# Performance work log

Hardware: AMD Instinct MI355X
Metric: run time of the kernel (lower is better)

The kernel has to match this reference:

```python
import jax, jax.numpy as jnp
import numpy as np

B_FACTOR = 4          # branching factor of the complete tree
DEPTH = 7             # levels 0..DEPTH; level DEPTH are leaves
N_NODES = (B_FACTOR ** (DEPTH + 1) - 1) // (B_FACTOR - 1)   # 21845
N_INTERNAL = (B_FACTOR ** DEPTH - 1) // (B_FACTOR - 1)      # 5461
IN_SIZE = 512
HID = 512
PARAM_SCALE = 0.02


def setup_inputs() -> dict:
    key = jax.random.key(0)
    ks = jax.random.split(key, 7)
    x = jax.random.normal(ks[0], (N_NODES, IN_SIZE), dtype=jnp.float32)
    # torch nn.Linear parameters: y = x @ W.T + b
    W_iou = jax.random.normal(ks[1], (3 * HID, IN_SIZE), dtype=jnp.float32) * PARAM_SCALE
    b_iou = jax.random.normal(ks[2], (3 * HID,), dtype=jnp.float32) * PARAM_SCALE
    W_f = jax.random.normal(ks[3], (HID, IN_SIZE), dtype=jnp.float32) * PARAM_SCALE
    b_f = jax.random.normal(ks[4], (HID,), dtype=jnp.float32) * PARAM_SCALE
    U_iou = jax.random.normal(ks[5], (3 * HID, HID), dtype=jnp.float32) * PARAM_SCALE
    U_f = jax.random.normal(ks[6], (HID, HID), dtype=jnp.float32) * PARAM_SCALE
    # children[j] = indices of the 4 children of internal node j (complete 4-ary tree)
    children = (B_FACTOR * jnp.arange(N_INTERNAL, dtype=jnp.int32)[:, None]
                + jnp.arange(1, B_FACTOR + 1, dtype=jnp.int32)[None, :])
    return {"x": x, "children": children, "W_iou": W_iou, "b_iou": b_iou,
            "W_f": W_f, "b_f": b_f, "U_iou": U_iou, "U_f": U_f}


def reference(x, children, W_iou, b_iou, W_f, b_f, U_iou, U_f):
    """Child-Sum Tree-LSTM over a complete 4-ary tree, processed level-batched
    bottom-up (equivalent to the per-node postorder recursion in the source).
    Leaves keep h = c = 0, as in the source (_forward_postorder returns early).
    NOTE: the source applies NO sigmoid to the forget gate term; we keep that.
    """
    N = x.shape[0]
    H = U_f.shape[0]
    # input-dependent parts are tree-independent: precompute once for all nodes
    wx_iou = x @ W_iou.T + b_iou          # [N, 3H]
    wx_f = x @ W_f.T + b_f                # [N, H]
    h = jnp.zeros((N, H), dtype=x.dtype)
    c = jnp.zeros_like(h)
    # level l occupies node indices [offs[l], offs[l+1]) — static constants
    offs = [(B_FACTOR ** l - 1) // (B_FACTOR - 1) for l in range(DEPTH + 2)]
    for l in range(DEPTH - 1, -1, -1):    # internal levels, deepest first
        s, e = offs[l], offs[l + 1]
        ch = children[s:e]                # [M, 4]
        h_ch = h[ch]                      # [M, 4, H] gather of child hidden states
        c_ch = c[ch]                      # [M, 4, H]
        h_sum = h_ch.sum(axis=1)          # child-sum
        iou = wx_iou[s:e] + h_sum @ U_iou.T               # [M, 3H]
        i, o, u = jnp.split(iou, 3, axis=-1)
        i = jax.nn.sigmoid(i)
        o = jax.nn.sigmoid(o)
        u = jnp.tanh(u)
        # forget term per child (no sigmoid, faithful to source)
        f = wx_f[s:e][:, None, :] + h_ch @ U_f.T          # [M, 4, H]
        c_new = i * u + (f * c_ch).sum(axis=1)            # [M, H]
        h = h.at[s:e].set(o * jnp.tanh(c_new))
        c = c.at[s:e].set(c_new)
    return h, c
```

## Files before the change

### kernel.cpp

```cpp
#include <hip/hip_runtime.h>
#include <cmath>

constexpr int N_NODES = 21845;
constexpr int N_INT   = 5461;
constexpr int HID     = 512;

typedef short  short8  __attribute__((ext_vector_type(8)));
typedef float  floatx4 __attribute__((ext_vector_type(4)));

__device__ __forceinline__ unsigned short f2bf(float f) {
    unsigned int u = __float_as_uint(f);
    u += 0x7fffu + ((u >> 16) & 1u);
    return (unsigned short)(u >> 16);
}

__global__ void prep_kernel(const float* __restrict__ x,
                            const float* __restrict__ W_iou,
                            const float* __restrict__ W_f,
                            const float* __restrict__ U_iou,
                            const float* __restrict__ U_f,
                            float* __restrict__ h_leaf,
                            float* __restrict__ c_leaf,
                            unsigned short* __restrict__ dstb,
                            unsigned* __restrict__ bar)
{
    if (blockIdx.x == 0 && threadIdx.x == 0) bar[0] = 0u;
    const size_t Z  = (size_t)(N_NODES - N_INT) * HID / 4;
    const size_t C0 = (size_t)N_INT * 512 / 4;
    const size_t C1 = C0 + 1536 * 512 / 4;
    const size_t C2 = C1 + 512 * 512 / 4;
    const size_t C3 = C2 + 1536 * 512 / 4;
    const size_t C4 = C3 + 512 * 512 / 4;
    const size_t total = 2 * Z + C4;
    size_t i = (size_t)blockIdx.x * blockDim.x + threadIdx.x;
    const size_t stride = (size_t)gridDim.x * blockDim.x;
    const float4 zz = {0.f, 0.f, 0.f, 0.f};
    for (; i < total; i += stride) {
        if (i < 2 * Z) {
            if (i < Z) ((float4*)h_leaf)[i] = zz;
            else       ((float4*)c_leaf)[i - Z] = zz;
        } else {
            size_t k = i - 2 * Z;
            const float* src; size_t off;
            if (k < C0)      { src = x;     off = k; }
            else if (k < C1) { src = W_iou; off = k - C0; }
            else if (k < C2) { src = W_f;   off = k - C1; }
            else if (k < C3) { src = U_iou; off = k - C2; }
            else             { src = U_f;   off = k - C3; }
            float4 v = ((const float4*)src)[off];
            ushort4 o;
            o.x = f2bf(v.x); o.y = f2bf(v.y); o.z = f2bf(v.z); o.w = f2bf(v.w);
            ((ushort4*)dstb)[k] = o;
        }
    }
}

#define GLD_LDS(g, l) __builtin_amdgcn_global_load_lds( \
    (const __attribute__((address_space(1))) void*)(g), \
    (__attribute__((address_space(3))) void*)(l), 16, 0, 0)

__device__ __forceinline__ void gemm_tile_128(
    const unsigned short* __restrict__ A, int Arows,
    const unsigned short* __restrict__ B,
    const float* __restrict__ bias,
    float* __restrict__ C, int ldc,
    int bm, int bn)
{
    __shared__ short8 AsV[1024];
    __shared__ short8 BsV[1024];

    const int tid  = threadIdx.x;
    const int wave = tid >> 6;
    const int lane = tid & 63;
    const int quad = lane >> 4;
    const int lr   = lane & 15;
    const int wr = (wave >> 1) * 64;
    const int wc = (wave & 1) * 64;

    floatx4 acc[4][4];
    #pragma unroll
    for (int i = 0; i < 4; ++i)
        #pragma unroll
        for (int j = 0; j < 4; ++j)
            acc[i][j] = (floatx4){0.f, 0.f, 0.f, 0.f};

    int s_row[4], s_gk[4];
    #pragma unroll
    for (int it = 0; it < 4; ++it) {
        int c = it * 256 + wave * 64 + lane;
        s_row[it] = c >> 3;
        s_gk[it]  = (c & 7) ^ (s_row[it] & 7);
    }

    for (int k0 = 0; k0 < 512; k0 += 64) {
        #pragma unroll
        for (int it = 0; it < 4; ++it) {
            int row = s_row[it];
            int gm = bm + row; if (gm >= Arows) gm = Arows - 1;
            GLD_LDS(A + (size_t)gm * 512 + k0 + s_gk[it] * 8, &AsV[it * 256 + wave * 64]);
            int gn = bn + row;
            GLD_LDS(B + (size_t)gn * 512 + k0 + s_gk[it] * 8, &BsV[it * 256 + wave * 64]);
        }
        __syncthreads();

        #pragma unroll
        for (int kc = 0; kc < 2; ++kc) {
            short8 af[4], bfr[4];
            const int q = kc * 4 + quad;
            #pragma unroll
            for (int mt = 0; mt < 4; ++mt) {
                int row = wr + mt * 16 + lr;
                af[mt] = AsV[row * 8 + (q ^ (row & 7))];
            }
            #pragma unroll
            for (int nt = 0; nt < 4; ++nt) {
                int row = wc + nt * 16 + lr;
                bfr[nt] = BsV[row * 8 + (q ^ (row & 7))];
            }
            #pragma unroll
            for (int mt = 0; mt < 4; ++mt)
                #pragma unroll
                for (int nt = 0; nt < 4; ++nt)
                    acc[mt][nt] = __builtin_amdgcn_mfma_f32_16x16x32_bf16(
                        af[mt], bfr[nt], acc[mt][nt], 0, 0, 0);
        }
        __syncthreads();
    }

    #pragma unroll
    for (int mt = 0; mt < 4; ++mt) {
        #pragma unroll
        for (int r = 0; r < 4; ++r) {
            int gm = bm + wr + mt * 16 + quad * 4 + r;
            if (gm >= Arows) continue;
            #pragma unroll
            for (int nt = 0; nt < 4; ++nt) {
                int gn = bn + wc + nt * 16 + lr;
                float v = acc[mt][nt][r];
                if (bias) v += bias[gn];
                C[(size_t)gm * ldc + gn] = v;
            }
        }
    }
}

__global__ __launch_bounds__(256) void wgemm_kernel(
    const unsigned short* __restrict__ xb,
    const unsigned short* __restrict__ Wib,
    const unsigned short* __restrict__ Wfb,
    const float* __restrict__ b_iou, const float* __restrict__ b_f,
    float* __restrict__ wx_iou, float* __restrict__ wx_f)
{
    int b = blockIdx.x;
    if (b < 516) {
        gemm_tile_128(xb, N_INT, Wib, b_iou, wx_iou, 1536, (b / 12) * 128, (b % 12) * 128);
    } else {
        int b2 = b - 516;
        gemm_tile_128(xb, 1365, Wfb, b_f, wx_f, 512, (b2 / 4) * 128, (b2 % 4) * 128);
    }
}

__global__ __launch_bounds__(256) void gemm5_kernel(
    const unsigned short* __restrict__ hs_bf,
    const unsigned short* __restrict__ h6_bf,
    const unsigned short* __restrict__ Uib, const unsigned short* __restrict__ Ufb,
    float* __restrict__ ioud, float* __restrict__ fd)
{
    int b = blockIdx.x;
    if (b < 96) {
        gemm_tile_128(hs_bf, 1024, Uib, nullptr, ioud, 1536, (b / 12) * 128, (b % 12) * 128);
    } else {
        int b2 = b - 96;
        gemm_tile_128(h6_bf, 4096, Ufb, nullptr, fd, 512, (b2 / 4) * 128, (b2 % 4) * 128);
    }
}

__global__ __launch_bounds__(512) void combine_wide_kernel(
    const float* __restrict__ wx_iou, const float* __restrict__ wx_f,
    const float* __restrict__ ioud, const float* __restrict__ fd,
    const float* __restrict__ c_child,
    float* __restrict__ h_out, float* __restrict__ c_out,
    unsigned short* __restrict__ h_bf, unsigned short* __restrict__ hs_bf,
    int s, int np)
{
    __shared__ float4 hsbuf[512];
    const int k  = threadIdx.x >> 7;
    const int jg = threadIdx.x & 127;
    const int j4 = jg << 2;
    const bool hasU = (ioud != nullptr);

    for (int tp = blockIdx.x; tp < np; tp += gridDim.x) {
        const int t = 4 * tp + k;
        const int n = s + t;
        const float* wrow = wx_iou + (size_t)n * 1536 + j4;
        float4 iv = *(const float4*)(wrow);
        float4 ov = *(const float4*)(wrow + 512);
        float4 uv = *(const float4*)(wrow + 1024);
        float4 fc = {0.f, 0.f, 0.f, 0.f};
        if (hasU) {
            const float* drow = ioud + (size_t)t * 1536 + j4;
            float4 a  = *(const float4*)(drow);
            float4 b  = *(const float4*)(drow + 512);
            float4 u2 = *(const float4*)(drow + 1024);
            float4 wf = *(const float4*)(wx_f + (size_t)n * 512 + j4);
            #pragma unroll
            for (int c = 0; c < 4; ++c) {
                ((float*)&iv)[c] += ((float*)&a)[c];
                ((float*)&ov)[c] += ((float*)&b)[c];
                ((float*)&uv)[c] += ((float*)&u2)[c];
            }
            #pragma unroll
            for (int q = 0; q < 4; ++q) {
                float4 f  = *(const float4*)(fd + (size_t)(4 * t + q) * 512 + j4);
                float4 cv = *(const float4*)(c_child + (size_t)(4 * t + q) * 512 + j4);
                #pragma unroll
                for (int c = 0; c < 4; ++c)
                    ((float*)&fc)[c] += (((float*)&wf)[c] + ((float*)&f)[c]) * ((float*)&cv)[c];
            }
        }
        float4 cn, hn; ushort4 hb;
        #pragma unroll
        for (int c = 0; c < 4; ++c) {
            float ig = 1.f / (1.f + expf(-((float*)&iv)[c]));
            float og = 1.f / (1.f + expf(-((float*)&ov)[c]));
            float ug = tanhf(((float*)&uv)[c]);
            float cv2 = ig * ug + ((float*)&fc)[c];
            float hv = og * tanhf(cv2);
            ((float*)&cn)[c] = cv2;
            ((float*)&hn)[c] = hv;
            ((unsigned short*)&hb)[c] = f2bf(hv);
        }
        *(float4*)(c_out + (size_t)n * 512 + j4) = cn;
        *(float4*)(h_out + (size_t)n * 512 + j4) = hn;
        *(ushort4*)(h_bf + (size_t)n * 512 + j4) = hb;
        hsbuf[threadIdx.x] = hn;
        __syncthreads();
        if (threadIdx.x < 128) {
            float4 s0 = hsbuf[jg], s1 = hsbuf[128 + jg], s2 = hsbuf[256 + jg], s3 = hsbuf[384 + jg];
            ushort4 ho;
            #pragma unroll
            for (int c = 0; c < 4; ++c)
                ((unsigned short*)&ho)[c] =
                    f2bf(((float*)&s0)[c] + ((float*)&s1)[c] + ((float*)&s2)[c] + ((float*)&s3)[c]);
            *(ushort4*)(hs_bf + (size_t)tp * 512 + j4) = ho;
        }
        __syncthreads();
    }
}

__device__ __forceinline__ void gbar(unsigned* bar, unsigned target) {
    __syncthreads();
    if (threadIdx.x == 0) {
        __threadfence();
        __hip_atomic_fetch_add(bar, 1u, __ATOMIC_RELEASE, __HIP_MEMORY_SCOPE_AGENT);
        while (__hip_atomic_load(bar, __ATOMIC_RELAXED, __HIP_MEMORY_SCOPE_AGENT) < target)
            __builtin_amdgcn_s_sleep(2);
        (void)__hip_atomic_load(bar, __ATOMIC_ACQUIRE, __HIP_MEMORY_SCOPE_AGENT);
    }
    __syncthreads();
}

__device__ void combine_level(
    const float* __restrict__ wx_iou, const float* __restrict__ wx_f,
    const float* __restrict__ ioud, const float* __restrict__ fd,
    const float* __restrict__ c_child,
    float* __restrict__ h_out, float* __restrict__ c_out,
    unsigned short* __restrict__ h_bf, unsigned short* __restrict__ hs_bf,
    int s, int nl)
{
    if (nl >= 4) {
        const int np = nl >> 2;
        const int total = np * 128;
        for (int idx = blockIdx.x * blockDim.x + threadIdx.x; idx < total;
             idx += gridDim.x * blockDim.x) {
            const int tp = idx >> 7;
            const int j4 = (idx & 127) << 2;
            float4 hs = {0.f, 0.f, 0.f, 0.f};
            #pragma unroll
            for (int k = 0; k < 4; ++k) {
                const int t = 4 * tp + k;
                const int n = s + t;
                const float* wrow = wx_iou + (size_t)n * 1536 + j4;
                float4 iv = *(const float4*)(wrow);
                float4 ov = *(const float4*)(wrow + 512);
                float4 uv = *(const float4*)(wrow + 1024);
                float4 fc = {0.f, 0.f, 0.f, 0.f};
                const float* drow = ioud + (size_t)t * 1536 + j4;
                float4 a  = *(const float4*)(drow);
                float4 b  = *(const float4*)(drow + 512);
                float4 u2 = *(const float4*)(drow + 1024);
                float4 wf = *(const float4*)(wx_f + (size_t)n * 512 + j4);
                #pragma unroll
                for (int c = 0; c < 4; ++c) {
                    ((float*)&iv)[c] += ((float*)&a)[c];
                    ((float*)&ov)[c] += ((float*)&b)[c];
                    ((float*)&uv)[c] += ((float*)&u2)[c];
                }
                #pragma unroll
                for (int q = 0; q < 4; ++q) {
                    float4 f  = *(const float4*)(fd + (size_t)(4 * t + q) * 512 + j4);
                    float4 cv = *(const float4*)(c_child + (size_t)(4 * t + q) * 512 + j4);
                    #pragma unroll
                    for (int c = 0; c < 4; ++c)
                        ((float*)&fc)[c] += (((float*)&wf)[c] + ((float*)&f)[c]) * ((float*)&cv)[c];
                }
                float4 cn, hn; ushort4 hb;
                #pragma unroll
                for (int c = 0; c < 4; ++c) {
                    float ig = 1.f / (1.f + expf(-((float*)&iv)[c]));
                    float og = 1.f / (1.f + expf(-((float*)&ov)[c]));
                    float ug = tanhf(((float*)&uv)[c]);
                    float cv2 = ig * ug + ((float*)&fc)[c];
                    float hv = og * tanhf(cv2);
                    ((float*)&cn)[c] = cv2;
                    ((float*)&hn)[c] = hv;
                    ((unsigned short*)&hb)[c] = f2bf(hv);
                    ((float*)&hs)[c] += hv;
                }
                *(float4*)(c_out + (size_t)n * 512 + j4) = cn;
                *(float4*)(h_out + (size_t)n * 512 + j4) = hn;
                *(ushort4*)(h_bf + (size_t)n * 512 + j4) = hb;
            }
            ushort4 ho;
            #pragma unroll
            for (int c = 0; c < 4; ++c) ((unsigned short*)&ho)[c] = f2bf(((float*)&hs)[c]);
            *(ushort4*)(hs_bf + (size_t)tp * 512 + j4) = ho;
        }
    } else {
        for (int idx = blockIdx.x * blockDim.x + threadIdx.x; idx < 128;
             idx += gridDim.x * blockDim.x) {
            const int j4 = idx << 2;
            const int n = s;
            const float* wrow = wx_iou + (size_t)n * 1536 + j4;
            float4 iv = *(const float4*)(wrow);
            float4 ov = *(const float4*)(wrow + 512);
            float4 uv = *(const float4*)(wrow + 1024);
            float4 a  = *(const float4*)(ioud + j4);
            float4 b  = *(const float4*)(ioud + 512 + j4);
            float4 u2 = *(const float4*)(ioud + 1024 + j4);
            float4 wf = *(const float4*)(wx_f + (size_t)n * 512 + j4);
            float4 fc = {0.f, 0.f, 0.f, 0.f};
            #pragma unroll
            for (int c = 0; c < 4; ++c) {
                ((float*)&iv)[c] += ((float*)&a)[c];
                ((float*)&ov)[c] += ((float*)&b)[c];
                ((float*)&uv)[c] += ((float*)&u2)[c];
            }
            #pragma unroll
            for (int q = 0; q < 4; ++q) {
                float4 f  = *(const float4*)(fd + (size_t)q * 512 + j4);
                float4 cv = *(const float4*)(c_child + (size_t)q * 512 + j4);
                #pragma unroll
                for (int c = 0; c < 4; ++c)
                    ((float*)&fc)[c] += (((float*)&wf)[c] + ((float*)&f)[c]) * ((float*)&cv)[c];
            }
            float4 cn, hn;
            #pragma unroll
            for (int c = 0; c < 4; ++c) {
                float ig = 1.f / (1.f + expf(-((float*)&iv)[c]));
                float og = 1.f / (1.f + expf(-((float*)&ov)[c]));
                float ug = tanhf(((float*)&uv)[c]);
                float cv2 = ig * ug + ((float*)&fc)[c];
                ((float*)&cn)[c] = cv2;
                ((float*)&hn)[c] = og * tanhf(cv2);
            }
            *(float4*)(c_out + (size_t)n * 512 + j4) = cn;
            *(float4*)(h_out + (size_t)n * 512 + j4) = hn;
        }
    }
}

__global__ __launch_bounds__(256) void tail_kernel(
    const float* __restrict__ wx_iou, const float* __restrict__ wx_f,
    const unsigned short* __restrict__ Uib, const unsigned short* __restrict__ Ufb,
    float* __restrict__ ioud, float* __restrict__ fd,
    float* __restrict__ h_out, float* __restrict__ c_out,
    unsigned short* __restrict__ h_bf, unsigned short* __restrict__ hs_bf,
    unsigned* __restrict__ bar)
{
    unsigned tgt = 0;
    const int offs[8] = {0, 1, 5, 21, 85, 341, 1365, 5461};
    for (int l = 4; l >= 0; --l) {
        const int s  = offs[l];
        const int nl = offs[l + 1] - s;
        const int cb = offs[l + 1];
        const int mI = (nl + 127) >> 7;
        const int mF = (4 * nl + 127) >> 7;
        const int nT = mI * 12 + mF * 4;

        for (int t = blockIdx.x; t < nT; t += gridDim.x) {
            if (t < mI * 12) {
                gemm_tile_128(hs_bf, nl, Uib, nullptr, ioud, 1536,
                              (t / 12) * 128, (t % 12) * 128);
            } else {
                int t2 = t - mI * 12;
                gemm_tile_128(h_bf + (size_t)cb * HID, 4 * nl, Ufb, nullptr, fd, 512,
                              (t2 / 4) * 128, (t2 % 4) * 128);
            }
        }
        tgt += gridDim.x; gbar(bar, tgt);

        combine_level(wx_iou, wx_f, ioud, fd, c_out + (size_t)cb * HID,
                      h_out, c_out, h_bf, hs_bf, s, nl);
        if (l > 0) { tgt += gridDim.x; gbar(bar, tgt); }
    }
}

extern "C" void kernel_launch(void* const* d_in, const int* in_sizes, int n_in,
                              void* d_out, int out_size, void* d_ws, size_t ws_size,
                              hipStream_t stream) {
    const float* x     = (const float*)d_in[0];
    const float* W_iou = (const float*)d_in[2];
    const float* b_iou = (const float*)d_in[3];
    const float* W_f   = (const float*)d_in[4];
    const float* b_f   = (const float*)d_in[5];
    const float* U_iou = (const float*)d_in[6];
    const float* U_f   = (const float*)d_in[7];

    float* h_out = (float*)d_out;
    float* c_out = h_out + (size_t)N_NODES * HID;

    float* ws     = (float*)d_ws;
    float* wx_iou = ws;
    float* wx_f   = wx_iou + (size_t)N_INT * 1536;
    float* ioud   = wx_f   + (size_t)1365 * 512;
    float* fd     = ioud   + (size_t)1024 * 1536;
    unsigned short* xb   = (unsigned short*)(fd + (size_t)4096 * 512);
    unsigned short* Wib  = xb  + (size_t)N_INT * 512;
    unsigned short* Wfb  = Wib + (size_t)1536 * 512;
    unsigned short* Uib  = Wfb + (size_t)512 * 512;
    unsigned short* Ufb  = Uib + (size_t)1536 * 512;
    unsigned short* h_bf = Ufb + (size_t)512 * 512;
    unsigned short* hs_bf= h_bf + (size_t)N_INT * 512;
    unsigned* bar = (unsigned*)(hs_bf + (size_t)1024 * 512);

    prep_kernel<<<2048, 256, 0, stream>>>(x, W_iou, W_f, U_iou, U_f,
                                          h_out + (size_t)N_INT * HID,
                                          c_out + (size_t)N_INT * HID,
                                          xb, bar);

    wgemm_kernel<<<516 + 44, 256, 0, stream>>>(xb, Wib, Wfb, b_iou, b_f, wx_iou, wx_f);

    combine_wide_kernel<<<1024, 512, 0, stream>>>(
        wx_iou, nullptr, nullptr, nullptr, nullptr,
        h_out, c_out, h_bf, hs_bf, 1365, 1024);

    gemm5_kernel<<<224, 256, 0, stream>>>(hs_bf, h_bf + (size_t)1365 * HID, Uib, Ufb, ioud, fd);

    combine_wide_kernel<<<256, 512, 0, stream>>>(
        wx_iou, wx_f, ioud, fd, c_out + (size_t)1365 * HID,
        h_out, c_out, h_bf, hs_bf, 341, 256);

    tail_kernel<<<128, 256, 0, stream>>>(wx_iou, wx_f, Uib, Ufb, ioud, fd,
                                         h_out, c_out, h_bf, hs_bf, bar);
}
```

Measured before the change: 325.1 us.

## Replace persistent tail kernel with per-level launches and small-tile MFMA GEMMs

```diff
diff --git a/kernel.cpp b/kernel.cpp
--- a/kernel.cpp
+++ b/kernel.cpp
@@ -21,10 +21,8 @@
                             const float* __restrict__ U_f,
                             float* __restrict__ h_leaf,
                             float* __restrict__ c_leaf,
-                            unsigned short* __restrict__ dstb,
-                            unsigned* __restrict__ bar)
-{
-    if (blockIdx.x == 0 && threadIdx.x == 0) bar[0] = 0u;
+                            unsigned short* __restrict__ dstb)
+{
     const size_t Z  = (size_t)(N_NODES - N_INT) * HID / 4;
     const size_t C0 = (size_t)N_INT * 512 / 4;
     const size_t C1 = C0 + 1536 * 512 / 4;
@@ -175,6 +173,77 @@
     }
 }
 
+__global__ __launch_bounds__(256) void gemm4_kernel(
+    const unsigned short* __restrict__ hs_bf,
+    const unsigned short* __restrict__ h5_bf,
+    const unsigned short* __restrict__ Uib, const unsigned short* __restrict__ Ufb,
+    float* __restrict__ ioud, float* __restrict__ fd)
+{
+    int b = blockIdx.x;
+    if (b < 24) {
+        gemm_tile_128(hs_bf, 256, Uib, nullptr, ioud, 1536, (b / 12) * 128, (b % 12) * 128);
+    } else {
+        int b2 = b - 24;
+        gemm_tile_128(h5_bf, 1024, Ufb, nullptr, fd, 512, (b2 / 4) * 128, (b2 % 4) * 128);
+    }
+}
+
+__device__ __forceinline__ void direct_tile_16x64(
+    const unsigned short* __restrict__ A, int Arows,
+    const unsigned short* __restrict__ B,
+    float* __restrict__ C, int ldc,
+    int m0, int n0)
+{
+    const int lane = threadIdx.x & 63;
+    const int quad = lane >> 4;
+    const int lr   = lane & 15;
+    int am = m0 + lr; if (am >= Arows) am = Arows - 1;
+    const unsigned short* ap = A + (size_t)am * 512 + quad * 8;
+    const unsigned short* bp = B + (size_t)(n0 + lr) * 512 + quad * 8;
+
+    floatx4 acc[4];
+    #pragma unroll
+    for (int j = 0; j < 4; ++j) acc[j] = (floatx4){0.f, 0.f, 0.f, 0.f};
+
+    #pragma unroll
+    for (int k0 = 0; k0 < 512; k0 += 32) {
+        short8 af = *(const short8*)(ap + k0);
+        #pragma unroll
+        for (int j = 0; j < 4; ++j) {
+            short8 bf = *(const short8*)(bp + (size_t)j * 16 * 512 + k0);
+            acc[j] = __builtin_amdgcn_mfma_f32_16x16x32_bf16(af, bf, acc[j], 0, 0, 0);
+        }
+    }
+
+    #pragma unroll
+    for (int j = 0; j < 4; ++j) {
+        #pragma unroll
+        for (int r = 0; r < 4; ++r) {
+            int gm = m0 + quad * 4 + r;
+            if (gm < Arows) C[(size_t)gm * ldc + n0 + j * 16 + lr] = acc[j][r];
+        }
+    }
+}
+
+__global__ __launch_bounds__(256) void gemm_small_kernel(
+    const unsigned short* __restrict__ hs_bf,
+    const unsigned short* __restrict__ hch_bf,
+    const unsigned short* __restrict__ Uib, const unsigned short* __restrict__ Ufb,
+    float* __restrict__ ioud, float* __restrict__ fd, int nl)
+{
+    const int w = blockIdx.x * 4 + (threadIdx.x >> 6);
+    const int mI = (nl + 15) >> 4;
+    const int nI = 1536 / 64;
+    const int mF = (4 * nl + 15) >> 4;
+    if (w < mI * nI) {
+        direct_tile_16x64(hs_bf, nl, Uib, ioud, 1536, (w / nI) * 16, (w % nI) * 64);
+    } else {
+        int w2 = w - mI * nI;
+        if (w2 < mF * 8)
+            direct_tile_16x64(hch_bf, 4 * nl, Ufb, fd, 512, (w2 / 8) * 16, (w2 % 8) * 64);
+    }
+}
+
 __global__ __launch_bounds__(512) void combine_wide_kernel(
     const float* __restrict__ wx_iou, const float* __restrict__ wx_f,
     const float* __restrict__ ioud, const float* __restrict__ fd,
@@ -248,162 +317,47 @@
     }
 }
 
-__device__ __forceinline__ void gbar(unsigned* bar, unsigned target) {
-    __syncthreads();
-    if (threadIdx.x == 0) {
-        __threadfence();
-        __hip_atomic_fetch_add(bar, 1u, __ATOMIC_RELEASE, __HIP_MEMORY_SCOPE_AGENT);
-        while (__hip_atomic_load(bar, __ATOMIC_RELAXED, __HIP_MEMORY_SCOPE_AGENT) < target)
-            __builtin_amdgcn_s_sleep(2);
-        (void)__hip_atomic_load(bar, __ATOMIC_ACQUIRE, __HIP_MEMORY_SCOPE_AGENT);
-    }
-    __syncthreads();
-}
-
-__device__ void combine_level(
+__global__ __launch_bounds__(128) void combine_root_kernel(
     const float* __restrict__ wx_iou, const float* __restrict__ wx_f,
     const float* __restrict__ ioud, const float* __restrict__ fd,
     const float* __restrict__ c_child,
-    float* __restrict__ h_out, float* __restrict__ c_out,
-    unsigned short* __restrict__ h_bf, unsigned short* __restrict__ hs_bf,
-    int s, int nl)
-{
-    if (nl >= 4) {
-        const int np = nl >> 2;
-        const int total = np * 128;
-        for (int idx = blockIdx.x * blockDim.x + threadIdx.x; idx < total;
-             idx += gridDim.x * blockDim.x) {
-            const int tp = idx >> 7;
-            const int j4 = (idx & 127) << 2;
-            float4 hs = {0.f, 0.f, 0.f, 0.f};
-            #pragma unroll
-            for (int k = 0; k < 4; ++k) {
-                const int t = 4 * tp + k;
-                const int n = s + t;
-                const float* wrow = wx_iou + (size_t)n * 1536 + j4;
-                float4 iv = *(const float4*)(wrow);
-                float4 ov = *(const float4*)(wrow + 512);
-                float4 uv = *(const float4*)(wrow + 1024);
-                float4 fc = {0.f, 0.f, 0.f, 0.f};
-                const float* drow = ioud + (size_t)t * 1536 + j4;
-                float4 a  = *(const float4*)(drow);
-                float4 b  = *(const float4*)(drow + 512);
-                float4 u2 = *(const float4*)(drow + 1024);
-                float4 wf = *(const float4*)(wx_f + (size_t)n * 512 + j4);
-                #pragma unroll
-                for (int c = 0; c < 4; ++c) {
-                    ((float*)&iv)[c] += ((float*)&a)[c];
-                    ((float*)&ov)[c] += ((float*)&b)[c];
-                    ((float*)&uv)[c] += ((float*)&u2)[c];
-                }
-                #pragma unroll
-                for (int q = 0; q < 4; ++q) {
-                    float4 f  = *(const float4*)(fd + (size_t)(4 * t + q) * 512 + j4);
-                    float4 cv = *(const float4*)(c_child + (size_t)(4 * t + q) * 512 + j4);
-                    #pragma unroll
-                    for (int c = 0; c < 4; ++c)
-                        ((float*)&fc)[c] += (((float*)&wf)[c] + ((float*)&f)[c]) * ((float*)&cv)[c];
-                }
-                float4 cn, hn; ushort4 hb;
-                #pragma unroll
-                for (int c = 0; c < 4; ++c) {
-                    float ig = 1.f / (1.f + expf(-((float*)&iv)[c]));
-                    float og = 1.f / (1.f + expf(-((float*)&ov)[c]));
-                    float ug = tanhf(((float*)&uv)[c]);
-                    float cv2 = ig * ug + ((float*)&fc)[c];
-                    float hv = og * tanhf(cv2);
-                    ((float*)&cn)[c] = cv2;
-                    ((float*)&hn)[c] = hv;
-                    ((unsigned short*)&hb)[c] = f2bf(hv);
-                    ((float*)&hs)[c] += hv;
-                }
-                *(float4*)(c_out + (size_t)n * 512 + j4) = cn;
-                *(float4*)(h_out + (size_t)n * 512 + j4) = hn;
-                *(ushort4*)(h_bf + (size_t)n * 512 + j4) = hb;
-            }
-            ushort4 ho;
-            #pragma unroll
-            for (int c = 0; c < 4; ++c) ((unsigned short*)&ho)[c] = f2bf(((float*)&hs)[c]);
-            *(ushort4*)(hs_bf + (size_t)tp * 512 + j4) = ho;
-        }
-    } else {
-        for (int idx = blockIdx.x * blockDim.x + threadIdx.x; idx < 128;
-             idx += gridDim.x * blockDim.x) {
-            const int j4 = idx << 2;
-            const int n = s;
-            const float* wrow = wx_iou + (size_t)n * 1536 + j4;
-            float4 iv = *(const float4*)(wrow);
-            float4 ov = *(const float4*)(wrow + 512);
-            float4 uv = *(const float4*)(wrow + 1024);
-            float4 a  = *(const float4*)(ioud + j4);
-            float4 b  = *(const float4*)(ioud + 512 + j4);
-            float4 u2 = *(const float4*)(ioud + 1024 + j4);
-            float4 wf = *(const float4*)(wx_f + (size_t)n * 512 + j4);
-            float4 fc = {0.f, 0.f, 0.f, 0.f};
-            #pragma unroll
-            for (int c = 0; c < 4; ++c) {
-                ((float*)&iv)[c] += ((float*)&a)[c];
-                ((float*)&ov)[c] += ((float*)&b)[c];
-                ((float*)&uv)[c] += ((float*)&u2)[c];
-            }
-            #pragma unroll
-            for (int q = 0; q < 4; ++q) {
-                float4 f  = *(const float4*)(fd + (size_t)q * 512 + j4);
-                float4 cv = *(const float4*)(c_child + (size_t)q * 512 + j4);
-                #pragma unroll
-                for (int c = 0; c < 4; ++c)
-                    ((float*)&fc)[c] += (((float*)&wf)[c] + ((float*)&f)[c]) * ((float*)&cv)[c];
-            }
-            float4 cn, hn;
-            #pragma unroll
-            for (int c = 0; c < 4; ++c) {
-                float ig = 1.f / (1.f + expf(-((float*)&iv)[c]));
-                float og = 1.f / (1.f + expf(-((float*)&ov)[c]));
-                float ug = tanhf(((float*)&uv)[c]);
-                float cv2 = ig * ug + ((float*)&fc)[c];
-                ((float*)&cn)[c] = cv2;
-                ((float*)&hn)[c] = og * tanhf(cv2);
-            }
-            *(float4*)(c_out + (size_t)n * 512 + j4) = cn;
-            *(float4*)(h_out + (size_t)n * 512 + j4) = hn;
-        }
-    }
-}
-
-__global__ __launch_bounds__(256) void tail_kernel(
-    const float* __restrict__ wx_iou, const float* __restrict__ wx_f,
-    const unsigned short* __restrict__ Uib, const unsigned short* __restrict__ Ufb,
-    float* __restrict__ ioud, float* __restrict__ fd,
-    float* __restrict__ h_out, float* __restrict__ c_out,
-    unsigned short* __restrict__ h_bf, unsigned short* __restrict__ hs_bf,
-    unsigned* __restrict__ bar)
-{
-    unsigned tgt = 0;
-    const int offs[8] = {0, 1, 5, 21, 85, 341, 1365, 5461};
-    for (int l = 4; l >= 0; --l) {
-        const int s  = offs[l];
-        const int nl = offs[l + 1] - s;
-        const int cb = offs[l + 1];
-        const int mI = (nl + 127) >> 7;
-        const int mF = (4 * nl + 127) >> 7;
-        const int nT = mI * 12 + mF * 4;
-
-        for (int t = blockIdx.x; t < nT; t += gridDim.x) {
-            if (t < mI * 12) {
-                gemm_tile_128(hs_bf, nl, Uib, nullptr, ioud, 1536,
-                              (t / 12) * 128, (t % 12) * 128);
-            } else {
-                int t2 = t - mI * 12;
-                gemm_tile_128(h_bf + (size_t)cb * HID, 4 * nl, Ufb, nullptr, fd, 512,
-                              (t2 / 4) * 128, (t2 % 4) * 128);
-            }
-        }
-        tgt += gridDim.x; gbar(bar, tgt);
-
-        combine_level(wx_iou, wx_f, ioud, fd, c_out + (size_t)cb * HID,
-                      h_out, c_out, h_bf, hs_bf, s, nl);
-        if (l > 0) { tgt += gridDim.x; gbar(bar, tgt); }
-    }
+    float* __restrict__ h_out, float* __restrict__ c_out)
+{
+    const int j4 = threadIdx.x << 2;
+    float4 iv = *(const float4*)(wx_iou + j4);
+    float4 ov = *(const float4*)(wx_iou + 512 + j4);
+    float4 uv = *(const float4*)(wx_iou + 1024 + j4);
+    float4 a  = *(const float4*)(ioud + j4);
+    float4 b  = *(const float4*)(ioud + 512 + j4);
+    float4 u2 = *(const float4*)(ioud + 1024 + j4);
+    float4 wf = *(const float4*)(wx_f + j4);
+    float4 fc = {0.f, 0.f, 0.f, 0.f};
+    #pragma unroll
+    for (int c = 0; c < 4; ++c) {
+        ((float*)&iv)[c] += ((float*)&a)[c];
+        ((float*)&ov)[c] += ((float*)&b)[c];
+        ((float*)&uv)[c] += ((float*)&u2)[c];
+    }
+    #pragma unroll
+    for (int q = 0; q < 4; ++q) {
+        float4 f  = *(const float4*)(fd + (size_t)q * 512 + j4);
+        float4 cv = *(const float4*)(c_child + (size_t)q * 512 + j4);
+        #pragma unroll
+        for (int c = 0; c < 4; ++c)
+            ((float*)&fc)[c] += (((float*)&wf)[c] + ((float*)&f)[c]) * ((float*)&cv)[c];
+    }
+    float4 cn, hn;
+    #pragma unroll
+    for (int c = 0; c < 4; ++c) {
+        float ig = 1.f / (1.f + expf(-((float*)&iv)[c]));
+        float og = 1.f / (1.f + expf(-((float*)&ov)[c]));
+        float ug = tanhf(((float*)&uv)[c]);
+        float cv2 = ig * ug + ((float*)&fc)[c];
+        ((float*)&cn)[c] = cv2;
+        ((float*)&hn)[c] = og * tanhf(cv2);
+    }
+    *(float4*)(c_out + j4) = cn;
+    *(float4*)(h_out + j4) = hn;
 }
 
 extern "C" void kernel_launch(void* const* d_in, const int* in_sizes, int n_in,
@@ -432,12 +386,12 @@
     unsigned short* Ufb  = Uib + (size_t)1536 * 512;
     unsigned short* h_bf = Ufb + (size_t)512 * 512;
     unsigned short* hs_bf= h_bf + (size_t)N_INT * 512;
-    unsigned* bar = (unsigned*)(hs_bf + (size_t)1024 * 512);
+
+    const int offs[9] = {0, 1, 5, 21, 85, 341, 1365, 5461, 21845};
 
     prep_kernel<<<2048, 256, 0, stream>>>(x, W_iou, W_f, U_iou, U_f,
                                           h_out + (size_t)N_INT * HID,
-                                          c_out + (size_t)N_INT * HID,
-                                          xb, bar);
+                                          c_out + (size_t)N_INT * HID, xb);
 
     wgemm_kernel<<<516 + 44, 256, 0, stream>>>(xb, Wib, Wfb, b_iou, b_f, wx_iou, wx_f);
 
@@ -446,11 +400,31 @@
         h_out, c_out, h_bf, hs_bf, 1365, 1024);
 
     gemm5_kernel<<<224, 256, 0, stream>>>(hs_bf, h_bf + (size_t)1365 * HID, Uib, Ufb, ioud, fd);
-
     combine_wide_kernel<<<256, 512, 0, stream>>>(
         wx_iou, wx_f, ioud, fd, c_out + (size_t)1365 * HID,
         h_out, c_out, h_bf, hs_bf, 341, 256);
 
-    tail_kernel<<<128, 256, 0, stream>>>(wx_iou, wx_f, Uib, Ufb, ioud, fd,
-                                         h_out, c_out, h_bf, hs_bf, bar);
-}
+    gemm4_kernel<<<56, 256, 0, stream>>>(hs_bf, h_bf + (size_t)341 * HID, Uib, Ufb, ioud, fd);
+    combine_wide_kernel<<<64, 512, 0, stream>>>(
+        wx_iou, wx_f, ioud, fd, c_out + (size_t)341 * HID,
+        h_out, c_out, h_bf, hs_bf, 85, 64);
+
+    for (int l = 3; l >= 1; --l) {
+        const int s  = offs[l];
+        const int nl = offs[l + 1] - s;
+        const int cb = offs[l + 1];
+        const int mI = (nl + 15) >> 4;
+        const int mF = (4 * nl + 15) >> 4;
+        const int waves = mI * 24 + mF * 8;
+        gemm_small_kernel<<<(waves + 3) / 4, 256, 0, stream>>>(
+            hs_bf, h_bf + (size_t)cb * HID, Uib, Ufb, ioud, fd, nl);
+        combine_wide_kernel<<<(nl + 3) / 4, 512, 0, stream>>>(
+            wx_iou, wx_f, ioud, fd, c_out + (size_t)cb * HID,
+            h_out, c_out, h_bf, hs_bf, s, nl >> 2);
+    }
+
+    gemm_small_kernel<<<8, 256, 0, stream>>>(
+        hs_bf, h_bf + (size_t)1 * HID, Uib, Ufb, ioud, fd, 1);
+    combine_root_kernel<<<1, 128, 0, stream>>>(
+        wx_iou, wx_f, ioud, fd, c_out + (size_t)1 * HID, h_out, c_out);
+}
```

Result: faster. 275.2 us (-15.3%).
